# Performance work log

Measured on AMD Instinct MI355X. Metric: run time of the kernel, lower is better.

## Reference

```python
import jax, jax.numpy as jnp
import numpy as np

T = 16384
IN = 14
H = 100
OUT = 1


def setup_inputs() -> dict:
    key = jax.random.key(0)
    ks = jax.random.split(key, 11)
    s_in = 1.0 / np.sqrt(H)
    x = jax.random.normal(ks[0], (T, IN), dtype=jnp.float32)
    # PyTorch nn.GRU params: weight_ih_l{k} [3H, in], weight_hh_l{k} [3H, H], biases [3H]; gate order (r, z, n)
    w_ih0 = jax.random.uniform(ks[1], (3 * H, IN), minval=-s_in, maxval=s_in, dtype=jnp.float32)
    w_hh0 = jax.random.uniform(ks[2], (3 * H, H), minval=-s_in, maxval=s_in, dtype=jnp.float32)
    b_ih0 = jax.random.uniform(ks[3], (3 * H,), minval=-s_in, maxval=s_in, dtype=jnp.float32)
    b_hh0 = jax.random.uniform(ks[4], (3 * H,), minval=-s_in, maxval=s_in, dtype=jnp.float32)
    w_ih1 = jax.random.uniform(ks[5], (3 * H, H), minval=-s_in, maxval=s_in, dtype=jnp.float32)
    w_hh1 = jax.random.uniform(ks[6], (3 * H, H), minval=-s_in, maxval=s_in, dtype=jnp.float32)
    b_ih1 = jax.random.uniform(ks[7], (3 * H,), minval=-s_in, maxval=s_in, dtype=jnp.float32)
    b_hh1 = jax.random.uniform(ks[8], (3 * H,), minval=-s_in, maxval=s_in, dtype=jnp.float32)
    fc_w = jax.random.uniform(ks[9], (OUT, H), minval=-s_in, maxval=s_in, dtype=jnp.float32)
    fc_b = jax.random.uniform(ks[10], (OUT,), minval=-s_in, maxval=s_in, dtype=jnp.float32)
    return {"x": x, "w_ih0": w_ih0, "w_hh0": w_hh0, "b_ih0": b_ih0, "b_hh0": b_hh0,
            "w_ih1": w_ih1, "w_hh1": w_hh1, "b_ih1": b_ih1, "b_hh1": b_hh1,
            "fc_w": fc_w, "fc_b": fc_b}


def _gru_layer(x_seq, w_ih, w_hh, b_ih, b_hh):
    # x_seq: [T, D_in] (batch=1 squeezed). Precompute input projections for all steps.
    gi = x_seq @ w_ih.T + b_ih  # [T, 3H]

    def step(h, gi_t):
        gh = h @ w_hh.T + b_hh  # [3H]
        i_r, i_z, i_n = jnp.split(gi_t, 3)
        h_r, h_z, h_n = jnp.split(gh, 3)
        r = jax.nn.sigmoid(i_r + h_r)
        z = jax.nn.sigmoid(i_z + h_z)
        n = jnp.tanh(i_n + r * h_n)
        h_new = (1.0 - z) * n + z * h
        return h_new, h_new

    h0 = jnp.zeros((w_hh.shape[1],), dtype=x_seq.dtype)
    _, out = jax.lax.scan(step, h0, gi)
    return out  # [T, H]


def reference(x, w_ih0, w_hh0, b_ih0, b_hh0, w_ih1, w_hh1, b_ih1, b_hh1, fc_w, fc_b):
    h1 = _gru_layer(x, w_ih0, w_hh0, b_ih0, b_hh0)   # layer 0: [T, H]
    h2 = _gru_layer(h1, w_ih1, w_hh1, b_ih1, b_hh1)  # layer 1: [T, H]
    out = h2 @ fc_w.T + fc_b                          # [T, 1]
    return out[-1]                                     # [1]
```

## Files before the change

kernel.cpp:

```cpp
#include <hip/hip_runtime.h>
#include <math.h>

#define T_STEPS 16384
#define IN_DIM  14
#define H_DIM   100
#define G_DIM   300
#define WPAD    116
#define WQ      29
#define SMEM_FLOATS (300*WPAD + 128 + 128 + 4*128)
#define SMEM_BYTES  (SMEM_FLOATS * 4)

typedef float f2 __attribute__((ext_vector_type(2)));
typedef float f4 __attribute__((ext_vector_type(4)));

__global__ void gi0_kernel(const float* __restrict__ x,
                           const float* __restrict__ w_ih0,
                           const float* __restrict__ b_ih0,
                           float* __restrict__ gi0) {
    int e = blockIdx.x * blockDim.x + threadIdx.x;
    if (e >= T_STEPS * G_DIM) return;
    int t = e / G_DIM;
    int j = e - t * G_DIM;
    const float* xr = x + t * IN_DIM;
    const float* wr = w_ih0 + j * IN_DIM;
    float acc = b_ih0[j];
    #pragma unroll
    for (int k = 0; k < IN_DIM; ++k) acc = fmaf(xr[k], wr[k], acc);
    gi0[e] = acc;
}

__global__ __launch_bounds__(384, 2)
void gru_lds_kernel(const float* __restrict__ gi0,
                    const float* __restrict__ w_hh0, const float* __restrict__ b_hh0,
                    const float* __restrict__ w_ih1, const float* __restrict__ b_ih1,
                    const float* __restrict__ w_hh1, const float* __restrict__ b_hh1,
                    const float* __restrict__ fc_w,  const float* __restrict__ fc_b,
                    float* __restrict__ out,
                    float* __restrict__ h1g, float* __restrict__ ag, int* flags) {
    extern __shared__ float smem[];
    float* w_s  = smem;
    float* bufA = smem + 300 * WPAD;
    float* bufB = bufA + 128;
    float* ring = bufB + 128;

    const int tid  = threadIdx.x;
    const int wave = tid >> 6;
    const int ln   = tid & 63;
    const int blk  = blockIdx.x;
    int* h1f = flags;
    int* af  = flags + 16;

    const float* Wsrc = (blk == 0) ? w_hh0 : (blk == 1) ? w_ih1 : w_hh1;
    for (int i = tid; i < 300 * 25; i += 384) {
        int r = i / 25, k = i - r * 25;
        reinterpret_cast<f4*>(w_s)[r * WQ + k] =
            reinterpret_cast<const f4*>(Wsrc + (size_t)r * H_DIM)[k];
    }
    if (tid < 128) { bufA[tid] = 0.0f; bufB[tid] = 0.0f; }

    const int ln20  = ln % 20;
    const int role  = ln / 20;
    const int roleC = (role > 2) ? 2 : role;
    const bool isR  = (role == 0);
    const int q     = wave * 20 + ln20;
    const int adZ   = (20 + ln20) << 2;
    const int adN   = (40 + ln20) << 2;

    if (blk == 0) {
        const int row = roleC * 100 + q;
        const f4* wr4 = reinterpret_cast<const f4*>(w_s) + row * WQ;
        float bias = (wave < 5) ? b_hh0[row] : 0.0f;

        float c_r = 0.f, c_z = 0.f, c_n = 0.f, n_r = 0.f, n_z = 0.f, n_n = 0.f;
        if (wave < 5 && isR) {
            const float* p = gi0 + q;
            c_r = p[0]; c_z = p[H_DIM]; c_n = p[2 * H_DIM];
        }
        __syncthreads();

        for (int t = 0; t <= T_STEPS; ++t) {
            float* bc = (t & 1) ? bufB : bufA;
            float* bn = (t & 1) ? bufA : bufB;
            if (wave < 5) {
                if (isR && t + 1 < T_STEPS) {
                    const float* p = gi0 + (size_t)(t + 1) * G_DIM + q;
                    n_r = p[0]; n_z = p[H_DIM]; n_n = p[2 * H_DIM];
                }
                float hold = isR ? bc[q] : 0.f;
                const f4* hb4 = reinterpret_cast<const f4*>(bc);
                f2 accA, accB;
                accA.x = bias; accA.y = 0.f; accB.x = 0.f; accB.y = 0.f;
                #pragma unroll
                for (int k = 0; k < 25; ++k) {
                    f4 H = hb4[k]; f4 W = wr4[k];
                    accA += W.lo * H.lo; accB += W.hi * H.hi;
                }
                float d  = (accA.x + accB.x) + (accA.y + accB.y);
                float dz = __int_as_float(__builtin_amdgcn_ds_bpermute(adZ, __float_as_int(d)));
                float dn = __int_as_float(__builtin_amdgcn_ds_bpermute(adN, __float_as_int(d)));
                if (isR && t < T_STEPS) {
                    float r = 1.0f / (1.0f + expf(-(c_r + d)));
                    float z = 1.0f / (1.0f + expf(-(c_z + dz)));
                    float n = tanhf(c_n + r * dn);
                    bn[q] = (1.0f - z) * n + z * hold;
                }
                c_r = n_r; c_z = n_z; c_n = n_n;
            } else if (wave == 5) {
                if (t >= 1) {
                    float* dst = h1g + (size_t)(t - 1) * H_DIM;
                    __hip_atomic_store(dst + ln, bc[ln], __ATOMIC_RELAXED, __HIP_MEMORY_SCOPE_AGENT);
                    if (ln < 36)
                        __hip_atomic_store(dst + 64 + ln, bc[64 + ln], __ATOMIC_RELAXED, __HIP_MEMORY_SCOPE_AGENT);
                    if ((t & 3) == 0 && ln == 0)
                        __hip_atomic_store(h1f, t, __ATOMIC_RELEASE, __HIP_MEMORY_SCOPE_AGENT);
                }
            }
            __syncthreads();
        }
    } else if (blk == 1) {
        const int rl  = (ln < 60) ? ln : 59;
        const int row = wave * 60 + rl;
        const f4* wr4 = reinterpret_cast<const f4*>(w_s) + row * WQ;
        float bias = (wave < 5) ? b_ih1[row] : 0.0f;
        int* myaf = af + wave * 16;

        int h1c = 0;
        float rA0 = 0.f, rA1 = 0.f;
        if (wave == 5) {
            while (h1c < 3)
                h1c = __hip_atomic_load(h1f, __ATOMIC_ACQUIRE, __HIP_MEMORY_SCOPE_AGENT);
            for (int e = 0; e < 2; ++e) {
                float* src = h1g + (size_t)e * H_DIM;
                float* dst = ring + e * 128;
                dst[ln] = __hip_atomic_load(src + ln, __ATOMIC_RELAXED, __HIP_MEMORY_SCOPE_AGENT);
                if (ln < 36)
                    dst[64 + ln] = __hip_atomic_load(src + 64 + ln, __ATOMIC_RELAXED, __HIP_MEMORY_SCOPE_AGENT);
            }
            rA0 = __hip_atomic_load(h1g + 2 * H_DIM + ln, __ATOMIC_RELAXED, __HIP_MEMORY_SCOPE_AGENT);
            if (ln < 36)
                rA1 = __hip_atomic_load(h1g + 2 * H_DIM + 64 + ln, __ATOMIC_RELAXED, __HIP_MEMORY_SCOPE_AGENT);
        }
        __syncthreads();

        for (int u = 0; u < T_STEPS; ++u) {
            if (wave < 5) {
                const f4* hb4 = reinterpret_cast<const f4*>(ring + (u & 3) * 128);
                f2 accA, accB;
                accA.x = bias; accA.y = 0.f; accB.x = 0.f; accB.y = 0.f;
                #pragma unroll
                for (int k = 0; k < 25; ++k) {
                    f4 H = hb4[k]; f4 W = wr4[k];
                    accA += W.lo * H.lo; accB += W.hi * H.hi;
                }
                float d = (accA.x + accB.x) + (accA.y + accB.y);
                if (ln < 60)
                    __hip_atomic_store(ag + (size_t)u * G_DIM + row, d, __ATOMIC_RELAXED, __HIP_MEMORY_SCOPE_AGENT);
                if ((u & 3) == 3 && ln == 0)
                    __hip_atomic_store(myaf, u + 1, __ATOMIC_RELEASE, __HIP_MEMORY_SCOPE_AGENT);
            } else if (wave == 5) {
                int ew = u + 2;
                if (ew < T_STEPS) {
                    float* dst = ring + (ew & 3) * 128;
                    dst[ln] = rA0;
                    if (ln < 36) dst[64 + ln] = rA1;
                }
                int el = u + 3;
                if (el < T_STEPS) {
                    while (h1c < el + 1)
                        h1c = __hip_atomic_load(h1f, __ATOMIC_ACQUIRE, __HIP_MEMORY_SCOPE_AGENT);
                    float* src = h1g + (size_t)el * H_DIM;
                    rA0 = __hip_atomic_load(src + ln, __ATOMIC_RELAXED, __HIP_MEMORY_SCOPE_AGENT);
                    if (ln < 36)
                        rA1 = __hip_atomic_load(src + 64 + ln, __ATOMIC_RELAXED, __HIP_MEMORY_SCOPE_AGENT);
                }
            }
            __syncthreads();
        }
    } else {
        const int row = roleC * 100 + q;
        const f4* wr4 = reinterpret_cast<const f4*>(w_s) + row * WQ;
        float bias = (wave < 5) ? b_hh1[row] : 0.0f;

        int am = 0;
        #define REFRESH(need) \
            while (am < (need)) { \
                int m0 = __hip_atomic_load(af +  0, __ATOMIC_ACQUIRE, __HIP_MEMORY_SCOPE_AGENT); \
                int m1 = __hip_atomic_load(af + 16, __ATOMIC_ACQUIRE, __HIP_MEMORY_SCOPE_AGENT); \
                int m2 = __hip_atomic_load(af + 32, __ATOMIC_ACQUIRE, __HIP_MEMORY_SCOPE_AGENT); \
                int m3 = __hip_atomic_load(af + 48, __ATOMIC_ACQUIRE, __HIP_MEMORY_SCOPE_AGENT); \
                int m4 = __hip_atomic_load(af + 64, __ATOMIC_ACQUIRE, __HIP_MEMORY_SCOPE_AGENT); \
                am = min(min(min(m0, m1), min(m2, m3)), m4); \
            }

        float c_r = 0.f, c_z = 0.f, c_n = 0.f, n_r = 0.f, n_z = 0.f, n_n = 0.f;
        if (wave < 5 && isR) {
            REFRESH(1);
            float* ap = ag + q;
            c_r = __hip_atomic_load(ap,             __ATOMIC_RELAXED, __HIP_MEMORY_SCOPE_AGENT);
            c_z = __hip_atomic_load(ap + H_DIM,     __ATOMIC_RELAXED, __HIP_MEMORY_SCOPE_AGENT);
            c_n = __hip_atomic_load(ap + 2 * H_DIM, __ATOMIC_RELAXED, __HIP_MEMORY_SCOPE_AGENT);
        }
        __syncthreads();

        for (int k2 = 0; k2 < T_STEPS; ++k2) {
            float* bc = (k2 & 1) ? bufB : bufA;
            float* bn = (k2 & 1) ? bufA : bufB;
            if (wave < 5) {
                if (isR && k2 + 1 < T_STEPS) {
                    REFRESH(k2 + 2);
                    float* ap = ag + (size_t)(k2 + 1) * G_DIM + q;
                    n_r = __hip_atomic_load(ap,             __ATOMIC_RELAXED, __HIP_MEMORY_SCOPE_AGENT);
                    n_z = __hip_atomic_load(ap + H_DIM,     __ATOMIC_RELAXED, __HIP_MEMORY_SCOPE_AGENT);
                    n_n = __hip_atomic_load(ap + 2 * H_DIM, __ATOMIC_RELAXED, __HIP_MEMORY_SCOPE_AGENT);
                }
                float hold = isR ? bc[q] : 0.f;
                const f4* hb4 = reinterpret_cast<const f4*>(bc);
                f2 accA, accB;
                accA.x = bias; accA.y = 0.f; accB.x = 0.f; accB.y = 0.f;
                #pragma unroll
                for (int k = 0; k < 25; ++k) {
                    f4 H = hb4[k]; f4 W = wr4[k];
                    accA += W.lo * H.lo; accB += W.hi * H.hi;
                }
                float d  = (accA.x + accB.x) + (accA.y + accB.y);
                float dz = __int_as_float(__builtin_amdgcn_ds_bpermute(adZ, __float_as_int(d)));
                float dn = __int_as_float(__builtin_amdgcn_ds_bpermute(adN, __float_as_int(d)));
                if (isR) {
                    float r = 1.0f / (1.0f + expf(-(c_r + d)));
                    float z = 1.0f / (1.0f + expf(-(c_z + dz)));
                    float n = tanhf(c_n + r * dn);
                    bn[q] = (1.0f - z) * n + z * hold;
                }
                c_r = n_r; c_z = n_z; c_n = n_n;
            }
            __syncthreads();
        }
        #undef REFRESH

        if (tid < 64) {
            float s = 0.0f;
            for (int j = tid; j < H_DIM; j += 64) s = fmaf(fc_w[j], bufA[j], s);
            #pragma unroll
            for (int off = 32; off > 0; off >>= 1) s += __shfl_down(s, off);
            if (tid == 0) out[0] = s + fc_b[0];
        }
    }
}

extern "C" void kernel_launch(void* const* d_in, const int* in_sizes, int n_in,
                              void* d_out, int out_size, void* d_ws, size_t ws_size,
                              hipStream_t stream) {
    const float* x     = (const float*)d_in[0];
    const float* w_ih0 = (const float*)d_in[1];
    const float* w_hh0 = (const float*)d_in[2];
    const float* b_ih0 = (const float*)d_in[3];
    const float* b_hh0 = (const float*)d_in[4];
    const float* w_ih1 = (const float*)d_in[5];
    const float* w_hh1 = (const float*)d_in[6];
    const float* b_ih1 = (const float*)d_in[7];
    const float* b_hh1 = (const float*)d_in[8];
    const float* fc_w  = (const float*)d_in[9];
    const float* fc_b  = (const float*)d_in[10];
    float* out = (float*)d_out;

    float* gi0 = (float*)d_ws;
    const size_t gi0_b = (size_t)T_STEPS * G_DIM * sizeof(float);
    float* h1g = (float*)((char*)d_ws + gi0_b);
    float* ag  = (float*)((char*)h1g + (size_t)T_STEPS * H_DIM * sizeof(float));
    int* flags = (int*)((char*)ag + (size_t)T_STEPS * G_DIM * sizeof(float));
    hipMemsetAsync(flags, 0, 512, stream);

    static bool attr_set = false;
    if (!attr_set) {
        hipFuncSetAttribute(reinterpret_cast<const void*>(&gru_lds_kernel),
                            hipFuncAttributeMaxDynamicSharedMemorySize, SMEM_BYTES);
        attr_set = true;
    }

    const int total = T_STEPS * G_DIM;
    gi0_kernel<<<(total + 255) / 256, 256, 0, stream>>>(x, w_ih0, b_ih0, gi0);
    gru_lds_kernel<<<3, 384, SMEM_BYTES, stream>>>(gi0, w_hh0, b_hh0, w_ih1, b_ih1,
                                                   w_hh1, b_hh1, fc_w, fc_b, out,
                                                   h1g, ag, flags);
}
```

Measured before the change: 18.90 ms.

## Keep GRU weights in registers and prefetch cross-block inputs via LDS rings

Each thread now keeps its 100-element weight row in VGPRs (50 float2 registers) instead of reading it from a padded LDS matrix every step, so the per-step dot product only reads the hidden state from LDS. Block 1 and block 2 now each use a dedicated wave that stages producer outputs (h1 rows, and the layer-1 input projections) into an 8-deep LDS ring about four steps ahead, replacing the per-thread global loads that sat on the critical path. Flag publication is also made more frequent so consumers see progress sooner. The cost is much higher register pressure under launch_bounds(384,2), which could cause spills, plus more frequent atomic flag stores.

New measurement: 21.34 ms. 1.13x slower.

```diff
diff --git a/kernel.cpp b/kernel.cpp
--- a/kernel.cpp
+++ b/kernel.cpp
@@ -5,13 +5,12 @@
 #define IN_DIM  14
 #define H_DIM   100
 #define G_DIM   300
-#define WPAD    116
-#define WQ      29
-#define SMEM_FLOATS (300*WPAD + 128 + 128 + 4*128)
-#define SMEM_BYTES  (SMEM_FLOATS * 4)
 
 typedef float f2 __attribute__((ext_vector_type(2)));
 typedef float f4 __attribute__((ext_vector_type(4)));
+
+#define REP25(M) M(0) M(1) M(2) M(3) M(4) M(5) M(6) M(7) M(8) M(9) M(10) M(11) \
+                 M(12) M(13) M(14) M(15) M(16) M(17) M(18) M(19) M(20) M(21) M(22) M(23) M(24)
 
 __global__ void gi0_kernel(const float* __restrict__ x,
                            const float* __restrict__ w_ih0,
@@ -30,18 +29,16 @@
 }
 
 __global__ __launch_bounds__(384, 2)
-void gru_lds_kernel(const float* __restrict__ gi0,
-                    const float* __restrict__ w_hh0, const float* __restrict__ b_hh0,
-                    const float* __restrict__ w_ih1, const float* __restrict__ b_ih1,
-                    const float* __restrict__ w_hh1, const float* __restrict__ b_hh1,
-                    const float* __restrict__ fc_w,  const float* __restrict__ fc_b,
-                    float* __restrict__ out,
-                    float* __restrict__ h1g, float* __restrict__ ag, int* flags) {
-    extern __shared__ float smem[];
-    float* w_s  = smem;
-    float* bufA = smem + 300 * WPAD;
-    float* bufB = bufA + 128;
-    float* ring = bufB + 128;
+void gru3_kernel(const float* __restrict__ gi0,
+                 const float* __restrict__ w_hh0, const float* __restrict__ b_hh0,
+                 const float* __restrict__ w_ih1, const float* __restrict__ b_ih1,
+                 const float* __restrict__ w_hh1, const float* __restrict__ b_hh1,
+                 const float* __restrict__ fc_w,  const float* __restrict__ fc_b,
+                 float* __restrict__ out,
+                 float* __restrict__ h1g, float* __restrict__ ag, int* flags) {
+    __shared__ __align__(16) float bufA[128];
+    __shared__ __align__(16) float bufB[128];
+    __shared__ __align__(16) float ring[8 * 304];
 
     const int tid  = threadIdx.x;
     const int wave = tid >> 6;
@@ -50,12 +47,6 @@
     int* h1f = flags;
     int* af  = flags + 16;
 
-    const float* Wsrc = (blk == 0) ? w_hh0 : (blk == 1) ? w_ih1 : w_hh1;
-    for (int i = tid; i < 300 * 25; i += 384) {
-        int r = i / 25, k = i - r * 25;
-        reinterpret_cast<f4*>(w_s)[r * WQ + k] =
-            reinterpret_cast<const f4*>(Wsrc + (size_t)r * H_DIM)[k];
-    }
     if (tid < 128) { bufA[tid] = 0.0f; bufB[tid] = 0.0f; }
 
     const int ln20  = ln % 20;
@@ -66,11 +57,25 @@
     const int adZ   = (20 + ln20) << 2;
     const int adN   = (40 + ln20) << 2;
 
+    #define DECLK(k) f2 wa_##k, wb_##k;
+    REP25(DECLK)
+    #undef DECLK
+    float bias = 0.0f;
+    {
+        const float* Wm; int row;
+        if (blk == 0)      { Wm = w_hh0; row = roleC * 100 + q; if (wave < 5) bias = b_hh0[row]; }
+        else if (blk == 1) { int rl = (ln < 60) ? ln : 59; Wm = w_ih1; row = wave * 60 + rl;
+                             if (wave < 5) bias = b_ih1[row]; }
+        else               { Wm = w_hh1; row = roleC * 100 + q; if (wave < 5) bias = b_hh1[row]; }
+        if (wave >= 5) row = 0;
+        const f4* p_ = reinterpret_cast<const f4*>(Wm + (size_t)row * H_DIM);
+        #define LOADK(k) { f4 V = p_[k]; wa_##k = V.lo; wb_##k = V.hi; }
+        REP25(LOADK)
+        #undef LOADK
+    }
+    #define DOTK(k) { f4 V = hb4_[k]; accA += wa_##k * V.lo; accB += wb_##k * V.hi; }
+
     if (blk == 0) {
-        const int row = roleC * 100 + q;
-        const f4* wr4 = reinterpret_cast<const f4*>(w_s) + row * WQ;
-        float bias = (wave < 5) ? b_hh0[row] : 0.0f;
-
         float c_r = 0.f, c_z = 0.f, c_n = 0.f, n_r = 0.f, n_z = 0.f, n_n = 0.f;
         if (wave < 5 && isR) {
             const float* p = gi0 + q;
@@ -87,14 +92,10 @@
                     n_r = p[0]; n_z = p[H_DIM]; n_n = p[2 * H_DIM];
                 }
                 float hold = isR ? bc[q] : 0.f;
-                const f4* hb4 = reinterpret_cast<const f4*>(bc);
+                const f4* hb4_ = reinterpret_cast<const f4*>(bc);
                 f2 accA, accB;
                 accA.x = bias; accA.y = 0.f; accB.x = 0.f; accB.y = 0.f;
-                #pragma unroll
-                for (int k = 0; k < 25; ++k) {
-                    f4 H = hb4[k]; f4 W = wr4[k];
-                    accA += W.lo * H.lo; accB += W.hi * H.hi;
-                }
+                REP25(DOTK)
                 float d  = (accA.x + accB.x) + (accA.y + accB.y);
                 float dz = __int_as_float(__builtin_amdgcn_ds_bpermute(adZ, __float_as_int(d)));
                 float dn = __int_as_float(__builtin_amdgcn_ds_bpermute(adN, __float_as_int(d)));
@@ -111,7 +112,7 @@
                     __hip_atomic_store(dst + ln, bc[ln], __ATOMIC_RELAXED, __HIP_MEMORY_SCOPE_AGENT);
                     if (ln < 36)
                         __hip_atomic_store(dst + 64 + ln, bc[64 + ln], __ATOMIC_RELAXED, __HIP_MEMORY_SCOPE_AGENT);
-                    if ((t & 3) == 0 && ln == 0)
+                    if ((t & 1) == 0 && ln == 0)
                         __hip_atomic_store(h1f, t, __ATOMIC_RELEASE, __HIP_MEMORY_SCOPE_AGENT);
                 }
             }
@@ -120,85 +121,68 @@
     } else if (blk == 1) {
         const int rl  = (ln < 60) ? ln : 59;
         const int row = wave * 60 + rl;
-        const f4* wr4 = reinterpret_cast<const f4*>(w_s) + row * WQ;
-        float bias = (wave < 5) ? b_ih1[row] : 0.0f;
-        int* myaf = af + wave * 16;
-
+        int* myaf = af + wave * 8;
         int h1c = 0;
-        float rA0 = 0.f, rA1 = 0.f;
+
         if (wave == 5) {
-            while (h1c < 3)
-                h1c = __hip_atomic_load(h1f, __ATOMIC_ACQUIRE, __HIP_MEMORY_SCOPE_AGENT);
-            for (int e = 0; e < 2; ++e) {
-                float* src = h1g + (size_t)e * H_DIM;
-                float* dst = ring + e * 128;
+            for (int e = 0; e < 4; ++e) {
+                while (h1c < e + 1)
+                    h1c = __hip_atomic_load(h1f, __ATOMIC_ACQUIRE, __HIP_MEMORY_SCOPE_AGENT);
+                const float* src = h1g + (size_t)e * H_DIM;
+                float* dst = ring + (e & 7) * 128;
                 dst[ln] = __hip_atomic_load(src + ln, __ATOMIC_RELAXED, __HIP_MEMORY_SCOPE_AGENT);
                 if (ln < 36)
                     dst[64 + ln] = __hip_atomic_load(src + 64 + ln, __ATOMIC_RELAXED, __HIP_MEMORY_SCOPE_AGENT);
             }
-            rA0 = __hip_atomic_load(h1g + 2 * H_DIM + ln, __ATOMIC_RELAXED, __HIP_MEMORY_SCOPE_AGENT);
-            if (ln < 36)
-                rA1 = __hip_atomic_load(h1g + 2 * H_DIM + 64 + ln, __ATOMIC_RELAXED, __HIP_MEMORY_SCOPE_AGENT);
         }
         __syncthreads();
 
         for (int u = 0; u < T_STEPS; ++u) {
             if (wave < 5) {
-                const f4* hb4 = reinterpret_cast<const f4*>(ring + (u & 3) * 128);
+                const f4* hb4_ = reinterpret_cast<const f4*>(ring + (u & 7) * 128);
                 f2 accA, accB;
                 accA.x = bias; accA.y = 0.f; accB.x = 0.f; accB.y = 0.f;
-                #pragma unroll
-                for (int k = 0; k < 25; ++k) {
-                    f4 H = hb4[k]; f4 W = wr4[k];
-                    accA += W.lo * H.lo; accB += W.hi * H.hi;
-                }
+                REP25(DOTK)
                 float d = (accA.x + accB.x) + (accA.y + accB.y);
                 if (ln < 60)
                     __hip_atomic_store(ag + (size_t)u * G_DIM + row, d, __ATOMIC_RELAXED, __HIP_MEMORY_SCOPE_AGENT);
-                if ((u & 3) == 3 && ln == 0)
+                if ((u & 1) == 1 && ln == 0)
                     __hip_atomic_store(myaf, u + 1, __ATOMIC_RELEASE, __HIP_MEMORY_SCOPE_AGENT);
             } else if (wave == 5) {
-                int ew = u + 2;
-                if (ew < T_STEPS) {
-                    float* dst = ring + (ew & 3) * 128;
-                    dst[ln] = rA0;
-                    if (ln < 36) dst[64 + ln] = rA1;
-                }
-                int el = u + 3;
-                if (el < T_STEPS) {
-                    while (h1c < el + 1)
+                const int e = u + 4;
+                if (e < T_STEPS) {
+                    while (h1c < e + 1)
                         h1c = __hip_atomic_load(h1f, __ATOMIC_ACQUIRE, __HIP_MEMORY_SCOPE_AGENT);
-                    float* src = h1g + (size_t)el * H_DIM;
-                    rA0 = __hip_atomic_load(src + ln, __ATOMIC_RELAXED, __HIP_MEMORY_SCOPE_AGENT);
+                    const float* src = h1g + (size_t)e * H_DIM;
+                    float* dst = ring + (e & 7) * 128;
+                    dst[ln] = __hip_atomic_load(src + ln, __ATOMIC_RELAXED, __HIP_MEMORY_SCOPE_AGENT);
                     if (ln < 36)
-                        rA1 = __hip_atomic_load(src + 64 + ln, __ATOMIC_RELAXED, __HIP_MEMORY_SCOPE_AGENT);
+                        dst[64 + ln] = __hip_atomic_load(src + 64 + ln, __ATOMIC_RELAXED, __HIP_MEMORY_SCOPE_AGENT);
                 }
             }
             __syncthreads();
         }
     } else {
-        const int row = roleC * 100 + q;
-        const f4* wr4 = reinterpret_cast<const f4*>(w_s) + row * WQ;
-        float bias = (wave < 5) ? b_hh1[row] : 0.0f;
-
         int am = 0;
-        #define REFRESH(need) \
-            while (am < (need)) { \
-                int m0 = __hip_atomic_load(af +  0, __ATOMIC_ACQUIRE, __HIP_MEMORY_SCOPE_AGENT); \
-                int m1 = __hip_atomic_load(af + 16, __ATOMIC_ACQUIRE, __HIP_MEMORY_SCOPE_AGENT); \
-                int m2 = __hip_atomic_load(af + 32, __ATOMIC_ACQUIRE, __HIP_MEMORY_SCOPE_AGENT); \
-                int m3 = __hip_atomic_load(af + 48, __ATOMIC_ACQUIRE, __HIP_MEMORY_SCOPE_AGENT); \
-                int m4 = __hip_atomic_load(af + 64, __ATOMIC_ACQUIRE, __HIP_MEMORY_SCOPE_AGENT); \
-                am = min(min(min(m0, m1), min(m2, m3)), m4); \
-            }
-
-        float c_r = 0.f, c_z = 0.f, c_n = 0.f, n_r = 0.f, n_z = 0.f, n_n = 0.f;
-        if (wave < 5 && isR) {
-            REFRESH(1);
-            float* ap = ag + q;
-            c_r = __hip_atomic_load(ap,             __ATOMIC_RELAXED, __HIP_MEMORY_SCOPE_AGENT);
-            c_z = __hip_atomic_load(ap + H_DIM,     __ATOMIC_RELAXED, __HIP_MEMORY_SCOPE_AGENT);
-            c_n = __hip_atomic_load(ap + 2 * H_DIM, __ATOMIC_RELAXED, __HIP_MEMORY_SCOPE_AGENT);
+        if (wave == 5) {
+            for (int e = 0; e < 4; ++e) {
+                while (am < e + 1) {
+                    int m0 = __hip_atomic_load(af +  0, __ATOMIC_ACQUIRE, __HIP_MEMORY_SCOPE_AGENT);
+                    int m1 = __hip_atomic_load(af +  8, __ATOMIC_ACQUIRE, __HIP_MEMORY_SCOPE_AGENT);
+                    int m2 = __hip_atomic_load(af + 16, __ATOMIC_ACQUIRE, __HIP_MEMORY_SCOPE_AGENT);
+                    int m3 = __hip_atomic_load(af + 24, __ATOMIC_ACQUIRE, __HIP_MEMORY_SCOPE_AGENT);
+                    int m4 = __hip_atomic_load(af + 32, __ATOMIC_ACQUIRE, __HIP_MEMORY_SCOPE_AGENT);
+                    am = min(min(min(m0, m1), min(m2, m3)), m4);
+                }
+                const float* src = ag + (size_t)e * G_DIM;
+                float* dst = ring + (e & 7) * 304;
+                dst[ln]       = __hip_atomic_load(src + ln,       __ATOMIC_RELAXED, __HIP_MEMORY_SCOPE_AGENT);
+                dst[64 + ln]  = __hip_atomic_load(src + 64 + ln,  __ATOMIC_RELAXED, __HIP_MEMORY_SCOPE_AGENT);
+                dst[128 + ln] = __hip_atomic_load(src + 128 + ln, __ATOMIC_RELAXED, __HIP_MEMORY_SCOPE_AGENT);
+                dst[192 + ln] = __hip_atomic_load(src + 192 + ln, __ATOMIC_RELAXED, __HIP_MEMORY_SCOPE_AGENT);
+                if (ln < 44)
+                    dst[256 + ln] = __hip_atomic_load(src + 256 + ln, __ATOMIC_RELAXED, __HIP_MEMORY_SCOPE_AGENT);
+            }
         }
         __syncthreads();
 
@@ -206,36 +190,48 @@
             float* bc = (k2 & 1) ? bufB : bufA;
             float* bn = (k2 & 1) ? bufA : bufB;
             if (wave < 5) {
-                if (isR && k2 + 1 < T_STEPS) {
-                    REFRESH(k2 + 2);
-                    float* ap = ag + (size_t)(k2 + 1) * G_DIM + q;
-                    n_r = __hip_atomic_load(ap,             __ATOMIC_RELAXED, __HIP_MEMORY_SCOPE_AGENT);
-                    n_z = __hip_atomic_load(ap + H_DIM,     __ATOMIC_RELAXED, __HIP_MEMORY_SCOPE_AGENT);
-                    n_n = __hip_atomic_load(ap + 2 * H_DIM, __ATOMIC_RELAXED, __HIP_MEMORY_SCOPE_AGENT);
-                }
-                float hold = isR ? bc[q] : 0.f;
-                const f4* hb4 = reinterpret_cast<const f4*>(bc);
+                float g_r = 0.f, g_z = 0.f, g_n = 0.f, hold = 0.f;
+                if (isR) {
+                    const float* ap = ring + (k2 & 7) * 304;
+                    g_r = ap[q]; g_z = ap[100 + q]; g_n = ap[200 + q];
+                    hold = bc[q];
+                }
+                const f4* hb4_ = reinterpret_cast<const f4*>(bc);
                 f2 accA, accB;
                 accA.x = bias; accA.y = 0.f; accB.x = 0.f; accB.y = 0.f;
-                #pragma unroll
-                for (int k = 0; k < 25; ++k) {
-                    f4 H = hb4[k]; f4 W = wr4[k];
-                    accA += W.lo * H.lo; accB += W.hi * H.hi;
-                }
+                REP25(DOTK)
                 float d  = (accA.x + accB.x) + (accA.y + accB.y);
                 float dz = __int_as_float(__builtin_amdgcn_ds_bpermute(adZ, __float_as_int(d)));
                 float dn = __int_as_float(__builtin_amdgcn_ds_bpermute(adN, __float_as_int(d)));
                 if (isR) {
-                    float r = 1.0f / (1.0f + expf(-(c_r + d)));
-                    float z = 1.0f / (1.0f + expf(-(c_z + dz)));
-                    float n = tanhf(c_n + r * dn);
+                    float r = 1.0f / (1.0f + expf(-(g_r + d)));
+                    float z = 1.0f / (1.0f + expf(-(g_z + dz)));
+                    float n = tanhf(g_n + r * dn);
                     bn[q] = (1.0f - z) * n + z * hold;
                 }
-                c_r = n_r; c_z = n_z; c_n = n_n;
+            } else if (wave == 5) {
+                const int e = k2 + 4;
+                if (e < T_STEPS) {
+                    while (am < e + 1) {
+                        int m0 = __hip_atomic_load(af +  0, __ATOMIC_ACQUIRE, __HIP_MEMORY_SCOPE_AGENT);
+                        int m1 = __hip_atomic_load(af +  8, __ATOMIC_ACQUIRE, __HIP_MEMORY_SCOPE_AGENT);
+                        int m2 = __hip_atomic_load(af + 16, __ATOMIC_ACQUIRE, __HIP_MEMORY_SCOPE_AGENT);
+                        int m3 = __hip_atomic_load(af + 24, __ATOMIC_ACQUIRE, __HIP_MEMORY_SCOPE_AGENT);
+                        int m4 = __hip_atomic_load(af + 32, __ATOMIC_ACQUIRE, __HIP_MEMORY_SCOPE_AGENT);
+                        am = min(min(min(m0, m1), min(m2, m3)), m4);
+                    }
+                    const float* src = ag + (size_t)e * G_DIM;
+                    float* dst = ring + (e & 7) * 304;
+                    dst[ln]       = __hip_atomic_load(src + ln,       __ATOMIC_RELAXED, __HIP_MEMORY_SCOPE_AGENT);
+                    dst[64 + ln]  = __hip_atomic_load(src + 64 + ln,  __ATOMIC_RELAXED, __HIP_MEMORY_SCOPE_AGENT);
+                    dst[128 + ln] = __hip_atomic_load(src + 128 + ln, __ATOMIC_RELAXED, __HIP_MEMORY_SCOPE_AGENT);
+                    dst[192 + ln] = __hip_atomic_load(src + 192 + ln, __ATOMIC_RELAXED, __HIP_MEMORY_SCOPE_AGENT);
+                    if (ln < 44)
+                        dst[256 + ln] = __hip_atomic_load(src + 256 + ln, __ATOMIC_RELAXED, __HIP_MEMORY_SCOPE_AGENT);
+                }
             }
             __syncthreads();
         }
-        #undef REFRESH
 
         if (tid < 64) {
             float s = 0.0f;
@@ -245,6 +241,7 @@
             if (tid == 0) out[0] = s + fc_b[0];
         }
     }
+    #undef DOTK
 }
 
 extern "C" void kernel_launch(void* const* d_in, const int* in_sizes, int n_in,
@@ -270,16 +267,9 @@
     int* flags = (int*)((char*)ag + (size_t)T_STEPS * G_DIM * sizeof(float));
     hipMemsetAsync(flags, 0, 512, stream);
 
-    static bool attr_set = false;
-    if (!attr_set) {
-        hipFuncSetAttribute(reinterpret_cast<const void*>(&gru_lds_kernel),
-                            hipFuncAttributeMaxDynamicSharedMemorySize, SMEM_BYTES);
-        attr_set = true;
-    }
-
     const int total = T_STEPS * G_DIM;
     gi0_kernel<<<(total + 255) / 256, 256, 0, stream>>>(x, w_ih0, b_ih0, gi0);
-    gru_lds_kernel<<<3, 384, SMEM_BYTES, stream>>>(gi0, w_hh0, b_hh0, w_ih1, b_ih1,
-                                                   w_hh1, b_hh1, fc_w, fc_b, out,
-                                                   h1g, ag, flags);
+    gru3_kernel<<<3, 384, 0, stream>>>(gi0, w_hh0, b_hh0, w_ih1, b_ih1,
+                                       w_hh1, b_hh1, fc_w, fc_b, out,
+                                       h1g, ag, flags);
 }
```
